# Kernel tuning notes

Hardware: AMD Instinct MI355X
Metric: run time of the kernel (lower is better)

## Reference

```python
import jax, jax.numpy as jnp
import numpy as np

B, S = 10000, 32        # batch nodes, sampled neighbors per node
N, D_IN, D_H = 100000, 512, 512


def setup_inputs() -> dict:
    key = jax.random.key(0)
    k1, k2, k3 = jax.random.split(key, 3)
    neigh_idx = jax.random.randint(k1, (B, S), 0, N)                 # int neighbor ids
    features = jax.random.normal(k2, (N, D_IN), dtype=jnp.float32)   # node feature table
    W = jax.random.normal(k3, (D_H, D_IN), dtype=jnp.float32) * (1.0 / np.sqrt(D_IN))
    b = jnp.zeros((D_H,), dtype=jnp.float32)
    return {"neigh_idx": neigh_idx, "features": features, "W": W, "b": b}


def reference(neigh_idx, features, W, b):
    # gather neighbor embeddings: [B, S, D_IN]
    neigh_feats = features[neigh_idx]
    # MLP: Linear(input_dim, hidden_dim) + ReLU  -> [B, S, D_H]
    h = jax.nn.relu(jnp.einsum("bsd,hd->bsh", neigh_feats, W) + b)
    # mask-based mean pool over sampled neighbors (mask @ embed / row_sum) -> [B, D_H]
    return jnp.mean(h, axis=1)
```

## Files before the change

### kernel.cpp

```cpp
#include <hip/hip_runtime.h>
#include <hip/hip_bf16.h>


#define S_NB 32
#define D_IN 512
#define D_H  512
#define BM   128
#define BN   128
#define BK   64
#define NNODE 100000
#define NBATCH 10000
#define NTILE_N (D_H / BN)
#define NTILE_M 784
#define NTILES  (NTILE_N * NTILE_M)

typedef __attribute__((ext_vector_type(8))) short  short8;
typedef __attribute__((ext_vector_type(4))) float  f32x4;
typedef __attribute__((ext_vector_type(4))) unsigned short us4;
typedef __attribute__((ext_vector_type(8))) unsigned short us8;

__device__ __forceinline__ unsigned short f2bf(float x) {
  union { float f; unsigned u; } v; v.f = x;
  unsigned r = v.u + 0x7FFFu + ((v.u >> 16) & 1u);
  return (unsigned short)(r >> 16);
}

__device__ __forceinline__ float bf2f(unsigned short x) {
  union { unsigned u; float f; } v; v.u = ((unsigned)x) << 16;
  return v.f;
}

__device__ __forceinline__ int swz(int row, int cb) {
  return row * 128 + (cb ^ ((row & 7) << 4));
}

__device__ __forceinline__ void gld_lds16(const unsigned short* g, unsigned short* l) {
  __builtin_amdgcn_global_load_lds(
      (const __attribute__((address_space(1))) unsigned int*)g,
      (__attribute__((address_space(3))) unsigned int*)l, 16, 0, 0);
}

__global__ __launch_bounds__(256, 8)
void cvt_bf16(const float* __restrict__ src, unsigned short* __restrict__ dst, int n8) {
  int i = blockIdx.x * blockDim.x + threadIdx.x;
  const int stride = gridDim.x * blockDim.x;
  for (; i < n8; i += stride) {
    f32x4 a = *(const f32x4*)(src + (size_t)i * 8);
    f32x4 b = *(const f32x4*)(src + (size_t)i * 8 + 4);
    us8 o;
    o[0] = f2bf(a.x); o[1] = f2bf(a.y); o[2] = f2bf(a.z); o[3] = f2bf(a.w);
    o[4] = f2bf(b.x); o[5] = f2bf(b.y); o[6] = f2bf(b.z); o[7] = f2bf(b.w);
    *(us8*)(dst + (size_t)i * 8) = o;
  }
}

__global__ __launch_bounds__(256, 4)
void gemm_hb(const unsigned short* __restrict__ featb,
             const unsigned short* __restrict__ Wb,
             const float* __restrict__ bias,
             unsigned short* __restrict__ Hb) {
  const int tid  = threadIdx.x;
  const int lane = tid & 63;
  const int wid  = tid >> 6;
  const int wr   = wid >> 1;
  const int wc   = wid & 1;

  const int bid  = blockIdx.x;
  const int tile = (bid & 7) * (NTILES / 8) + (bid >> 3);
  const int n0   = (tile & 3) * BN;
  const int m0   = (tile >> 2) * BM;

  __shared__ __align__(16) unsigned short smem[BM * BK * 2];
  unsigned short* As = smem;
  unsigned short* Bs = smem + BM * BK;

  const unsigned short* srcA[4];
  const unsigned short* srcB[4];
  unsigned short* dstA[4];
  unsigned short* dstB[4];
#pragma unroll
  for (int i = 0; i < 4; ++i) {
    int rl = wid * 32 + i * 8 + (lane >> 3);
    int g  = (lane & 7) ^ (rl & 7);
    int ra = m0 + rl; if (ra > NNODE - 1) ra = NNODE - 1;
    srcA[i] = featb + (size_t)ra * D_IN + g * 8;
    srcB[i] = Wb + (size_t)(n0 + rl) * D_IN + g * 8;
    dstA[i] = As + (wid * 32 + i * 8) * 64;
    dstB[i] = Bs + (wid * 32 + i * 8) * 64;
  }

  f32x4 acc[4][4];
#pragma unroll
  for (int i = 0; i < 4; ++i)
#pragma unroll
    for (int j = 0; j < 4; ++j)
      acc[i][j] = (f32x4){0.f, 0.f, 0.f, 0.f};

  const int frow = lane & 15;
  const int kcb  = (lane >> 4) * 16;
  const int arow = wr * 64 + frow;
  const int brow = wc * 64 + frow;

  for (int ki = 0; ki < D_IN / BK; ++ki) {
    const int k0 = ki * BK;
    if (ki) __syncthreads();
#pragma unroll
    for (int i = 0; i < 4; ++i) {
      gld_lds16(srcA[i] + k0, dstA[i]);
      gld_lds16(srcB[i] + k0, dstB[i]);
    }
    __syncthreads();

#pragma unroll
    for (int kk = 0; kk < 2; ++kk) {
      short8 af[4], bfr[4];
#pragma unroll
      for (int mi = 0; mi < 4; ++mi)
        af[mi] = *(const short8*)((const char*)As + swz(arow + mi * 16, kk * 64 + kcb));
#pragma unroll
      for (int ni = 0; ni < 4; ++ni)
        bfr[ni] = *(const short8*)((const char*)Bs + swz(brow + ni * 16, kk * 64 + kcb));
#pragma unroll
      for (int mi = 0; mi < 4; ++mi)
#pragma unroll
        for (int ni = 0; ni < 4; ++ni)
          acc[mi][ni] = __builtin_amdgcn_mfma_f32_16x16x32_bf16(af[mi], bfr[ni], acc[mi][ni], 0, 0, 0);
    }
  }

  __syncthreads();
  unsigned short* Cs = smem;
  const int rq = lane >> 4;
#pragma unroll
  for (int ni = 0; ni < 4; ++ni) {
    int col = wc * 64 + ni * 16 + frow;
    float bv = bias[n0 + col];
#pragma unroll
    for (int mi = 0; mi < 4; ++mi) {
#pragma unroll
      for (int r = 0; r < 4; ++r) {
        int row = wr * 64 + mi * 16 + rq * 4 + r;
        Cs[row * 128 + col] = f2bf(fmaxf(acc[mi][ni][r] + bv, 0.f));
      }
    }
  }
  __syncthreads();

  const int srow = tid >> 4;
  const int scol = (tid & 15) * 8;
#pragma unroll
  for (int it = 0; it < 8; ++it) {
    int row  = it * 16 + srow;
    int grow = m0 + row;
    us8 v = *(const us8*)(Cs + row * 128 + scol);
    if (grow < NNODE)
      *(us8*)(Hb + (size_t)grow * D_H + n0 + scol) = v;
  }
}

__global__ __launch_bounds__(256, 8)
void pool_mean(const unsigned short* __restrict__ Hb,
               const int* __restrict__ nidx,
               float* __restrict__ out) {
  const int b2   = blockIdx.x;
  const int half = threadIdx.x >> 7;
  const int t    = threadIdx.x & 127;
  const int b    = b2 * 2 + half;

  __shared__ int rows[2][S_NB];
  if (threadIdx.x < 2 * S_NB)
    rows[threadIdx.x >> 5][threadIdx.x & 31] = nidx[b2 * 2 * S_NB + threadIdx.x];
  __syncthreads();

  const int c = t * 4;
  float s0 = 0.f, s1 = 0.f, s2 = 0.f, s3 = 0.f;
#pragma unroll
  for (int s = 0; s < S_NB; ++s) {
    us4 v = *(const us4*)(Hb + (size_t)rows[half][s] * D_H + c);
    s0 += bf2f(v.x); s1 += bf2f(v.y); s2 += bf2f(v.z); s3 += bf2f(v.w);
  }
  f32x4 o; o.x = s0 * (1.0f / S_NB); o.y = s1 * (1.0f / S_NB);
  o.z = s2 * (1.0f / S_NB); o.w = s3 * (1.0f / S_NB);
  *(f32x4*)(out + (size_t)b * D_H + c) = o;
}

__global__ __launch_bounds__(256, 4)
void gemm_h(const float* __restrict__ feat,
            const float* __restrict__ Wm,
            const float* __restrict__ bias,
            unsigned short* __restrict__ Hb) {
  const int tid  = threadIdx.x;
  const int lane = tid & 63;
  const int wid  = tid >> 6;
  const int wr   = wid >> 1;
  const int wc   = wid & 1;
  const int n0   = blockIdx.x * BN;
  const int m0   = blockIdx.y * BM;

  __shared__ __align__(16) unsigned short As[BM * BK];
  __shared__ __align__(16) unsigned short Bs[BM * BK];

  const int lr = tid >> 4;
  const int lc = tid & 15;

  const float* aptr[8];
  const float* wptr[8];
#pragma unroll
  for (int p = 0; p < 8; ++p) {
    int row = p * 16 + lr;
    int gr  = m0 + row; if (gr > NNODE - 1) gr = NNODE - 1;
    aptr[p] = feat + (size_t)gr * D_IN + lc * 4;
    wptr[p] = Wm + (size_t)(n0 + row) * D_IN + lc * 4;
  }

  f32x4 acc[4][4];
#pragma unroll
  for (int i = 0; i < 4; ++i)
#pragma unroll
    for (int j = 0; j < 4; ++j)
      acc[i][j] = (f32x4){0.f, 0.f, 0.f, 0.f};

  const int frow = lane & 15;
  const int kcb  = (lane >> 4) * 16;
  const int arow = wr * 64 + frow;
  const int brow = wc * 64 + frow;

  for (int k0 = 0; k0 < D_IN; k0 += BK) {
    __syncthreads();
#pragma unroll
    for (int p = 0; p < 8; ++p) {
      int row = p * 16 + lr;
      f32x4 av = *(const f32x4*)(aptr[p] + k0);
      f32x4 wv = *(const f32x4*)(wptr[p] + k0);
      us4 a4, w4;
      a4.x = f2bf(av.x); a4.y = f2bf(av.y); a4.z = f2bf(av.z); a4.w = f2bf(av.w);
      w4.x = f2bf(wv.x); w4.y = f2bf(wv.y); w4.z = f2bf(wv.z); w4.w = f2bf(wv.w);
      *(us4*)((char*)As + swz(row, lc * 8)) = a4;
      *(us4*)((char*)Bs + swz(row, lc * 8)) = w4;
    }
    __syncthreads();

#pragma unroll
    for (int kk = 0; kk < 2; ++kk) {
      short8 af[4], bfr[4];
#pragma unroll
      for (int mi = 0; mi < 4; ++mi)
        af[mi] = *(const short8*)((const char*)As + swz(arow + mi * 16, kk * 64 + kcb));
#pragma unroll
      for (int ni = 0; ni < 4; ++ni)
        bfr[ni] = *(const short8*)((const char*)Bs + swz(brow + ni * 16, kk * 64 + kcb));
#pragma unroll
      for (int mi = 0; mi < 4; ++mi)
#pragma unroll
        for (int ni = 0; ni < 4; ++ni)
          acc[mi][ni] = __builtin_amdgcn_mfma_f32_16x16x32_bf16(af[mi], bfr[ni], acc[mi][ni], 0, 0, 0);
    }
  }

  const int rq = lane >> 4;
#pragma unroll
  for (int ni = 0; ni < 4; ++ni) {
    int col = n0 + wc * 64 + ni * 16 + frow;
    float bv = bias[col];
#pragma unroll
    for (int mi = 0; mi < 4; ++mi) {
#pragma unroll
      for (int r = 0; r < 4; ++r) {
        int grow = m0 + wr * 64 + mi * 16 + rq * 4 + r;
        if (grow < NNODE)
          Hb[(size_t)grow * D_H + col] = f2bf(fmaxf(acc[mi][ni][r] + bv, 0.f));
      }
    }
  }
}

__global__ __launch_bounds__(256, 4)
void pool_aggr_gemm(const int* __restrict__ nidx_g,
                    const float* __restrict__ feat,
                    const float* __restrict__ Wm,
                    const float* __restrict__ bias,
                    float* __restrict__ out) {
  const int tid  = threadIdx.x;
  const int lane = tid & 63;
  const int wid  = tid >> 6;
  const int wr   = wid >> 1;
  const int wc   = wid & 1;
  const int n0   = blockIdx.x * BN;
  const int mb   = blockIdx.y;

  __shared__ __align__(16) unsigned short As[BM * BK];
  __shared__ __align__(16) unsigned short Bs[BM * BK];
  __shared__ int nid[BM];

  if (tid < BM) nid[tid] = nidx_g[mb * BM + tid];
  __syncthreads();

  const int lr = tid >> 4;
  const int lc = tid & 15;

  const float* aptr[8];
  const float* wptr[8];
#pragma unroll
  for (int p = 0; p < 8; ++p) {
    int row = p * 16 + lr;
    aptr[p] = feat + (size_t)nid[row] * D_IN + lc * 4;
    wptr[p] = Wm + (size_t)(n0 + row) * D_IN + lc * 4;
  }

  f32x4 acc[4][4];
#pragma unroll
  for (int i = 0; i < 4; ++i)
#pragma unroll
    for (int j = 0; j < 4; ++j)
      acc[i][j] = (f32x4){0.f, 0.f, 0.f, 0.f};

  const int frow = lane & 15;
  const int kcb  = (lane >> 4) * 16;
  const int arow = wr * 64 + frow;
  const int brow = wc * 64 + frow;

  for (int k0 = 0; k0 < D_IN; k0 += BK) {
    __syncthreads();
#pragma unroll
    for (int p = 0; p < 8; ++p) {
      int row = p * 16 + lr;
      f32x4 av = *(const f32x4*)(aptr[p] + k0);
      f32x4 wv = *(const f32x4*)(wptr[p] + k0);
      us4 a4, w4;
      a4.x = f2bf(av.x); a4.y = f2bf(av.y); a4.z = f2bf(av.z); a4.w = f2bf(av.w);
      w4.x = f2bf(wv.x); w4.y = f2bf(wv.y); w4.z = f2bf(wv.z); w4.w = f2bf(wv.w);
      *(us4*)((char*)As + swz(row, lc * 8)) = a4;
      *(us4*)((char*)Bs + swz(row, lc * 8)) = w4;
    }
    __syncthreads();

#pragma unroll
    for (int kk = 0; kk < 2; ++kk) {
      short8 af[4], bfr[4];
#pragma unroll
      for (int mi = 0; mi < 4; ++mi)
        af[mi] = *(const short8*)((const char*)As + swz(arow + mi * 16, kk * 64 + kcb));
#pragma unroll
      for (int ni = 0; ni < 4; ++ni)
        bfr[ni] = *(const short8*)((const char*)Bs + swz(brow + ni * 16, kk * 64 + kcb));
#pragma unroll
      for (int mi = 0; mi < 4; ++mi)
#pragma unroll
        for (int ni = 0; ni < 4; ++ni)
          acc[mi][ni] = __builtin_amdgcn_mfma_f32_16x16x32_bf16(af[mi], bfr[ni], acc[mi][ni], 0, 0, 0);
    }
  }

  const int rq = lane >> 4;
#pragma unroll
  for (int ni = 0; ni < 4; ++ni) {
    int col = n0 + wc * 64 + ni * 16 + frow;
    float bv = bias[col];
#pragma unroll
    for (int bl = 0; bl < 2; ++bl) {
      float s = 0.f;
#pragma unroll
      for (int m2 = 0; m2 < 2; ++m2) {
        int mi = bl * 2 + m2;
#pragma unroll
        for (int r = 0; r < 4; ++r)
          s += fmaxf(acc[mi][ni][r] + bv, 0.f);
      }
      s += __shfl_xor(s, 16);
      s += __shfl_xor(s, 32);
      if (rq == 0) {
        int bb = mb * 4 + wr * 2 + bl;
        out[(size_t)bb * D_H + col] = s * (1.0f / (float)S_NB);
      }
    }
  }
}

extern "C" void kernel_launch(void* const* d_in, const int* in_sizes, int n_in,
                              void* d_out, int out_size, void* d_ws, size_t ws_size,
                              hipStream_t stream) {
  const int*   nidx = (const int*)d_in[0];
  const float* feat = (const float*)d_in[1];
  const float* Wm   = (const float*)d_in[2];
  const float* bias = (const float*)d_in[3];
  float* out = (float*)d_out;

  const size_t featb_bytes = (size_t)NNODE * D_IN * sizeof(unsigned short);
  const size_t wb_bytes    = (size_t)D_H * D_IN * sizeof(unsigned short);
  const size_t h_bytes     = (size_t)NNODE * D_H * sizeof(unsigned short);

  if (ws_size >= featb_bytes + wb_bytes + h_bytes) {
    unsigned short* featb = (unsigned short*)d_ws;
    unsigned short* Wb    = featb + (size_t)NNODE * D_IN;
    unsigned short* Hb    = Wb + (size_t)D_H * D_IN;

    cvt_bf16<<<2048, 256, 0, stream>>>(feat, featb, NNODE * D_IN / 8);
    cvt_bf16<<<128, 256, 0, stream>>>(Wm, Wb, D_H * D_IN / 8);
    gemm_hb<<<NTILES, 256, 0, stream>>>(featb, Wb, bias, Hb);
    pool_mean<<<NBATCH / 2, 256, 0, stream>>>(Hb, nidx, out);
  } else if (ws_size >= h_bytes) {
    unsigned short* Hb = (unsigned short*)d_ws;
    dim3 g1(D_H / BN, (NNODE + BM - 1) / BM);
    gemm_h<<<g1, 256, 0, stream>>>(feat, Wm, bias, Hb);
    pool_mean<<<NBATCH / 2, 256, 0, stream>>>(Hb, nidx, out);
  } else {
    dim3 grid(D_H / BN, NBATCH / 4);
    pool_aggr_gemm<<<grid, 256, 0, stream>>>(nidx, feat, Wm, bias, out);
  }
}
```

Measured before the change: 197.1 us.

## Fuse fp32-to-bf16 feature conversion into double-buffered GEMM and widen pooling loads

Drops the separate feature conversion pass. The GEMM now reads fp32 features directly, converts them to bf16 in registers, and writes them into a double-buffered LDS tile while the MFMAs on the current tile run. This removes a full write and re-read of the bf16 feature table. The cost is double the LDS use and more register pressure, with launch bounds lowered to 2 blocks per CU. The pooling kernel also moves to 4 batch rows per block with 16-byte loads per thread.

```diff
diff --git a/kernel.cpp b/kernel.cpp
--- a/kernel.cpp
+++ b/kernel.cpp
@@ -10,7 +10,7 @@
 #define BK   64
 #define NNODE 100000
 #define NBATCH 10000
-#define NTILE_N (D_H / BN)
+#define NTILE_N 4
 #define NTILE_M 784
 #define NTILES  (NTILE_N * NTILE_M)
 
@@ -54,8 +54,8 @@
   }
 }
 
-__global__ __launch_bounds__(256, 4)
-void gemm_hb(const unsigned short* __restrict__ featb,
+__global__ __launch_bounds__(256, 2)
+void gemm_hf(const float* __restrict__ feat,
              const unsigned short* __restrict__ Wb,
              const float* __restrict__ bias,
              unsigned short* __restrict__ Hb) {
@@ -70,23 +70,29 @@
   const int n0   = (tile & 3) * BN;
   const int m0   = (tile >> 2) * BM;
 
-  __shared__ __align__(16) unsigned short smem[BM * BK * 2];
-  unsigned short* As = smem;
-  unsigned short* Bs = smem + BM * BK;
-
-  const unsigned short* srcA[4];
-  const unsigned short* srcB[4];
-  unsigned short* dstA[4];
-  unsigned short* dstB[4];
+  __shared__ __align__(16) unsigned short As[2][BM * BK];
+  __shared__ __align__(16) unsigned short Bs[2][BM * BK];
+
+  const int lr = tid >> 4;
+  const int lc = tid & 15;
+  const float* aptr[8];
+  int awoff[8];
+#pragma unroll
+  for (int p = 0; p < 8; ++p) {
+    int row = p * 16 + lr;
+    int gr  = m0 + row; if (gr > NNODE - 1) gr = NNODE - 1;
+    aptr[p]  = feat + (size_t)gr * D_IN + lc * 4;
+    awoff[p] = swz(row, lc * 8);
+  }
+
+  const unsigned short* srcW[4];
+  int wdoff[4];
 #pragma unroll
   for (int i = 0; i < 4; ++i) {
     int rl = wid * 32 + i * 8 + (lane >> 3);
     int g  = (lane & 7) ^ (rl & 7);
-    int ra = m0 + rl; if (ra > NNODE - 1) ra = NNODE - 1;
-    srcA[i] = featb + (size_t)ra * D_IN + g * 8;
-    srcB[i] = Wb + (size_t)(n0 + rl) * D_IN + g * 8;
-    dstA[i] = As + (wid * 32 + i * 8) * 64;
-    dstB[i] = Bs + (wid * 32 + i * 8) * 64;
+    srcW[i]  = Wb + (size_t)(n0 + rl) * D_IN + g * 8;
+    wdoff[i] = (wid * 32 + i * 8) * 64;
   }
 
   f32x4 acc[4][4];
@@ -101,35 +107,61 @@
   const int arow = wr * 64 + frow;
   const int brow = wc * 64 + frow;
 
+  {
+    f32x4 a0[8];
+#pragma unroll
+    for (int p = 0; p < 8; ++p) a0[p] = *(const f32x4*)(aptr[p]);
+#pragma unroll
+    for (int i = 0; i < 4; ++i) gld_lds16(srcW[i], &Bs[0][wdoff[i]]);
+#pragma unroll
+    for (int p = 0; p < 8; ++p) {
+      us4 v;
+      v.x = f2bf(a0[p].x); v.y = f2bf(a0[p].y); v.z = f2bf(a0[p].z); v.w = f2bf(a0[p].w);
+      *(us4*)((char*)As[0] + awoff[p]) = v;
+    }
+  }
+  __syncthreads();
+
+#pragma unroll
   for (int ki = 0; ki < D_IN / BK; ++ki) {
-    const int k0 = ki * BK;
-    if (ki) __syncthreads();
-#pragma unroll
-    for (int i = 0; i < 4; ++i) {
-      gld_lds16(srcA[i] + k0, dstA[i]);
-      gld_lds16(srcB[i] + k0, dstB[i]);
-    }
-    __syncthreads();
+    const int cur = ki & 1;
+
+    f32x4 an[8];
+    if (ki < D_IN / BK - 1) {
+#pragma unroll
+      for (int p = 0; p < 8; ++p) an[p] = *(const f32x4*)(aptr[p] + (ki + 1) * BK);
+#pragma unroll
+      for (int i = 0; i < 4; ++i) gld_lds16(srcW[i] + (ki + 1) * BK, &Bs[cur ^ 1][wdoff[i]]);
+    }
 
 #pragma unroll
     for (int kk = 0; kk < 2; ++kk) {
       short8 af[4], bfr[4];
 #pragma unroll
       for (int mi = 0; mi < 4; ++mi)
-        af[mi] = *(const short8*)((const char*)As + swz(arow + mi * 16, kk * 64 + kcb));
+        af[mi] = *(const short8*)((const char*)As[cur] + swz(arow + mi * 16, kk * 64 + kcb));
 #pragma unroll
       for (int ni = 0; ni < 4; ++ni)
-        bfr[ni] = *(const short8*)((const char*)Bs + swz(brow + ni * 16, kk * 64 + kcb));
+        bfr[ni] = *(const short8*)((const char*)Bs[cur] + swz(brow + ni * 16, kk * 64 + kcb));
 #pragma unroll
       for (int mi = 0; mi < 4; ++mi)
 #pragma unroll
         for (int ni = 0; ni < 4; ++ni)
           acc[mi][ni] = __builtin_amdgcn_mfma_f32_16x16x32_bf16(af[mi], bfr[ni], acc[mi][ni], 0, 0, 0);
     }
-  }
-
-  __syncthreads();
-  unsigned short* Cs = smem;
+
+    if (ki < D_IN / BK - 1) {
+#pragma unroll
+      for (int p = 0; p < 8; ++p) {
+        us4 v;
+        v.x = f2bf(an[p].x); v.y = f2bf(an[p].y); v.z = f2bf(an[p].z); v.w = f2bf(an[p].w);
+        *(us4*)((char*)As[cur ^ 1] + awoff[p]) = v;
+      }
+    }
+    __syncthreads();
+  }
+
+  unsigned short* Cs = &As[0][0];
   const int rq = lane >> 4;
 #pragma unroll
   for (int ni = 0; ni < 4; ++ni) {
@@ -159,29 +191,33 @@
 }
 
 __global__ __launch_bounds__(256, 8)
-void pool_mean(const unsigned short* __restrict__ Hb,
-               const int* __restrict__ nidx,
-               float* __restrict__ out) {
-  const int b2   = blockIdx.x;
-  const int half = threadIdx.x >> 7;
-  const int t    = threadIdx.x & 127;
-  const int b    = b2 * 2 + half;
-
-  __shared__ int rows[2][S_NB];
-  if (threadIdx.x < 2 * S_NB)
-    rows[threadIdx.x >> 5][threadIdx.x & 31] = nidx[b2 * 2 * S_NB + threadIdx.x];
+void pool_mean4(const unsigned short* __restrict__ Hb,
+                const int* __restrict__ nidx,
+                float* __restrict__ out) {
+  const int b4 = blockIdx.x;
+  const int q  = threadIdx.x >> 6;
+  const int t  = threadIdx.x & 63;
+  const int b  = b4 * 4 + q;
+
+  __shared__ int rows[4][S_NB];
+  if (threadIdx.x < 4 * S_NB)
+    rows[threadIdx.x >> 5][threadIdx.x & 31] = nidx[b4 * 4 * S_NB + threadIdx.x];
   __syncthreads();
 
-  const int c = t * 4;
+  const int c = t * 8;
   float s0 = 0.f, s1 = 0.f, s2 = 0.f, s3 = 0.f;
+  float s4 = 0.f, s5 = 0.f, s6 = 0.f, s7 = 0.f;
 #pragma unroll
   for (int s = 0; s < S_NB; ++s) {
-    us4 v = *(const us4*)(Hb + (size_t)rows[half][s] * D_H + c);
-    s0 += bf2f(v.x); s1 += bf2f(v.y); s2 += bf2f(v.z); s3 += bf2f(v.w);
-  }
-  f32x4 o; o.x = s0 * (1.0f / S_NB); o.y = s1 * (1.0f / S_NB);
-  o.z = s2 * (1.0f / S_NB); o.w = s3 * (1.0f / S_NB);
-  *(f32x4*)(out + (size_t)b * D_H + c) = o;
+    us8 v = *(const us8*)(Hb + (size_t)rows[q][s] * D_H + c);
+    s0 += bf2f(v[0]); s1 += bf2f(v[1]); s2 += bf2f(v[2]); s3 += bf2f(v[3]);
+    s4 += bf2f(v[4]); s5 += bf2f(v[5]); s6 += bf2f(v[6]); s7 += bf2f(v[7]);
+  }
+  const float inv = 1.0f / (float)S_NB;
+  f32x4 o1; o1.x = s0 * inv; o1.y = s1 * inv; o1.z = s2 * inv; o1.w = s3 * inv;
+  f32x4 o2; o2.x = s4 * inv; o2.y = s5 * inv; o2.z = s6 * inv; o2.w = s7 * inv;
+  *(f32x4*)(out + (size_t)b * D_H + c)     = o1;
+  *(f32x4*)(out + (size_t)b * D_H + c + 4) = o2;
 }
 
 __global__ __launch_bounds__(256, 4)
@@ -385,24 +421,21 @@
   const float* bias = (const float*)d_in[3];
   float* out = (float*)d_out;
 
-  const size_t featb_bytes = (size_t)NNODE * D_IN * sizeof(unsigned short);
-  const size_t wb_bytes    = (size_t)D_H * D_IN * sizeof(unsigned short);
-  const size_t h_bytes     = (size_t)NNODE * D_H * sizeof(unsigned short);
-
-  if (ws_size >= featb_bytes + wb_bytes + h_bytes) {
-    unsigned short* featb = (unsigned short*)d_ws;
-    unsigned short* Wb    = featb + (size_t)NNODE * D_IN;
-    unsigned short* Hb    = Wb + (size_t)D_H * D_IN;
-
-    cvt_bf16<<<2048, 256, 0, stream>>>(feat, featb, NNODE * D_IN / 8);
+  const size_t wb_elems = (size_t)D_H * D_IN;
+  const size_t wb_bytes = wb_elems * sizeof(unsigned short);
+  const size_t h_bytes  = (size_t)NNODE * D_H * sizeof(unsigned short);
+
+  if (ws_size >= wb_bytes + h_bytes) {
+    unsigned short* Wb = (unsigned short*)d_ws;
+    unsigned short* Hb = Wb + wb_elems;
     cvt_bf16<<<128, 256, 0, stream>>>(Wm, Wb, D_H * D_IN / 8);
-    gemm_hb<<<NTILES, 256, 0, stream>>>(featb, Wb, bias, Hb);
-    pool_mean<<<NBATCH / 2, 256, 0, stream>>>(Hb, nidx, out);
+    gemm_hf<<<NTILES, 256, 0, stream>>>(feat, Wb, bias, Hb);
+    pool_mean4<<<NBATCH / 4, 256, 0, stream>>>(Hb, nidx, out);
   } else if (ws_size >= h_bytes) {
     unsigned short* Hb = (unsigned short*)d_ws;
     dim3 g1(D_H / BN, (NNODE + BM - 1) / BM);
     gemm_h<<<g1, 256, 0, stream>>>(feat, Wm, bias, Hb);
-    pool_mean<<<NBATCH / 2, 256, 0, stream>>>(Hb, nidx, out);
+    pool_mean4<<<NBATCH / 4, 256, 0, stream>>>(Hb, nidx, out);
   } else {
     dim3 grid(D_H / BN, NBATCH / 4);
     pool_aggr_gemm<<<grid, 256, 0, stream>>>(nidx, feat, Wm, bias, out);
```

Result: faster. 192.2 us (-2.5%).
